# Optimization experiments

Hardware: AMD Instinct MI355X
Metric: run time of the kernel (lower is better)

Reference implementation:

```python
import jax, jax.numpy as jnp
import numpy as np

EPS = 1e-5

def conv1x1_bn(x, W, b, gamma, beta, mean, var):
    # x: (B,C,H,W); W: (O,C) 1x1 conv; BN in eval mode with running stats
    y = jnp.einsum('bchw,oc->bohw', x, W) + b[None, :, None, None]
    scale = gamma / jnp.sqrt(var + EPS)
    return y * scale[None, :, None, None] + (beta - mean * scale)[None, :, None, None]

def setup_inputs() -> dict:
    key = jax.random.key(0)
    ks = jax.random.split(key, 12)
    B, C, H, W = 8, 64, 128, 256
    d = {
        'fea_left': jax.random.normal(ks[0], (B, C, H, W), jnp.float32),
        'fea_right': jax.random.normal(ks[1], (B, C, H, W), jnp.float32),
        'Wq': jax.random.normal(ks[2], (C, C), jnp.float32) * (1.0 / np.sqrt(C)),
        'bq': jax.random.normal(ks[3], (C,), jnp.float32) * 0.02,
        'gq': 1.0 + 0.1 * jax.random.normal(ks[4], (C,), jnp.float32),
        'betaq': 0.02 * jax.random.normal(ks[5], (C,), jnp.float32),
        'mq': 0.02 * jax.random.normal(ks[6], (C,), jnp.float32),
        'vq': jax.random.uniform(ks[7], (C,), jnp.float32, 0.5, 1.5),
        'Wk': jax.random.normal(ks[8], (C, C), jnp.float32) * (1.0 / np.sqrt(C)),
        'bk': jax.random.normal(ks[9], (C,), jnp.float32) * 0.02,
        'gk': 1.0 + 0.1 * jax.random.normal(ks[10], (C,), jnp.float32),
        'betak': 0.02 * jax.random.normal(ks[11], (C,), jnp.float32),
        'mk': 0.02 * jax.random.normal(jax.random.fold_in(key, 100), (C,), jnp.float32),
        'vk': jax.random.uniform(jax.random.fold_in(key, 101), (C,), jnp.float32, 0.5, 1.5),
    }
    return d

def _attend(src, tgt, Wq, bq, gq, betaq, mq, vq, Wk, bk, gk, betak, mk, vk):
    # query from src, key from tgt, values are raw tgt features
    c = src.shape[1]
    Q = conv1x1_bn(src, Wq, bq, gq, betaq, mq, vq)   # (B,C,H,W)
    K = conv1x1_bn(tgt, Wk, bk, gk, betak, mk, vk)   # (B,C,H,W)
    # cost: (B,H,Wq,Wk) = Q^T K over channels, per image row
    cost = jnp.einsum('bchw,bchv->bhwv', Q, K) / c
    attn = jax.nn.softmax(cost, axis=-1)
    out = jnp.einsum('bhwv,bchv->bchw', attn, tgt)   # back to (B,C,H,W)
    return out

def reference(fea_left, fea_right, Wq, bq, gq, betaq, mq, vq, Wk, bk, gk, betak, mk, vk):
    cxr = _attend(fea_left, fea_right, Wq, bq, gq, betaq, mq, vq, Wk, bk, gk, betak, mk, vk)
    enh = _attend(fea_right, fea_left, Wq, bq, gq, betaq, mq, vq, Wk, bk, gk, betak, mk, vk)
    return (cxr, enh)
```

## Files before the change

kernel.cpp:

```cpp
#include <hip/hip_runtime.h>

#define HW_ 32768
#define OUTHALF 16777216ULL
#define SMEM_BYTES 117760

typedef short short8  __attribute__((ext_vector_type(8)));
typedef short short4v __attribute__((ext_vector_type(4)));
typedef float f32x4   __attribute__((ext_vector_type(4)));

__device__ __forceinline__ unsigned short f2bf(float f) {
  unsigned u = __builtin_bit_cast(unsigned, f);
  u += 0x7fffu + ((u >> 16) & 1u);
  return (unsigned short)(u >> 16);
}
__device__ __forceinline__ float bf2f(short s) {
  unsigned u = ((unsigned)(unsigned short)s) << 16;
  return __builtin_bit_cast(float, u);
}
__device__ __forceinline__ char* swz(char* base, int row, int colByte) {
  return base + row * 128 + (colByte ^ ((row & 7) << 4));
}
__device__ __forceinline__ f32x4 zero4() { f32x4 z = {0.f, 0.f, 0.f, 0.f}; return z; }

__global__ void pam_setup(const float* __restrict__ Wq, const float* __restrict__ bq,
                          const float* __restrict__ gq, const float* __restrict__ betaq,
                          const float* __restrict__ mq, const float* __restrict__ vq,
                          const float* __restrict__ Wk, const float* __restrict__ gk,
                          const float* __restrict__ vk,
                          short* __restrict__ Mbt, float* __restrict__ u) {
  int blk = blockIdx.x, tid = threadIdx.x;
  if (blk < 16) {
    int entry = blk * 256 + tid;
    int y = entry >> 6, x = entry & 63;
    float acc = 0.f;
    for (int o = 0; o < 64; ++o) {
      float sq = gq[o] * rsqrtf(vq[o] + 1e-5f);
      float sk = gk[o] * rsqrtf(vk[o] + 1e-5f);
      acc += Wq[o * 64 + x] * sq * Wk[o * 64 + y] * sk;
    }
    Mbt[y * 64 + x] = (short)f2bf(acc);
  } else if (tid < 64) {
    int y = tid;
    float acc = 0.f;
    for (int o = 0; o < 64; ++o) {
      float sq = gq[o] * rsqrtf(vq[o] + 1e-5f);
      float sk = gk[o] * rsqrtf(vk[o] + 1e-5f);
      float bqq = bq[o] * sq + betaq[o] - mq[o] * sq;
      acc += bqq * Wk[o * 64 + y] * sk;
    }
    u[y] = acc;
  }
}

__global__ __launch_bounds__(1024, 4) void pam_main(
    const float* __restrict__ fl, const float* __restrict__ fr,
    const short* __restrict__ Mbt, const float* __restrict__ uvec,
    float* __restrict__ out) {
  extern __shared__ __align__(16) char sm[];
  char* XLt = sm;
  char* XRt = sm + 32768;
  char* Xn0 = sm + 65536;
  char* Pt  = sm + 81920;
  float* tl = (float*)(sm + 114688);
  float* Db = (float*)(sm + 116736);

  const int tid  = threadIdx.x;
  const int lane = tid & 63;
  const int wave = tid >> 6;
  const int l15  = lane & 15;
  const int g    = lane >> 4;
  const int bb   = blockIdx.x >> 7;
  const int hh   = blockIdx.x & 127;
  const int rowOff = hh * 256;
  const int base_b = bb * 64;
  const int w0   = wave * 16;

  char* Ptw = Pt + wave * 2048;

  #pragma unroll
  for (int it = 0; it < 8; ++it) {
    int unit = it * 1024 + tid;
    int tensor = unit >> 12;
    int rem = unit & 4095;
    int cq = rem >> 8;
    int p  = rem & 255;
    const float* s = (tensor ? fr : fl) + (size_t)(base_b + cq * 4) * HW_ + rowOff + p;
    float v0 = s[0], v1 = s[HW_], v2 = s[2 * HW_], v3 = s[3 * HW_];
    short4v pk;
    pk[0] = (short)f2bf(v0); pk[1] = (short)f2bf(v1);
    pk[2] = (short)f2bf(v2); pk[3] = (short)f2bf(v3);
    *(short4v*)swz(tensor ? XRt : XLt, p, cq * 8) = pk;
  }
  __syncthreads();

  if (tid < 512) {
    int sel = tid >> 8, p = tid & 255;
    char* xt = sel ? XLt : XRt;
    float acc = 0.f;
    #pragma unroll
    for (int j = 0; j < 8; ++j) {
      short8 xv = *(const short8*)swz(xt, p, j * 16);
      #pragma unroll
      for (int e = 0; e < 8; ++e)
        acc = fmaf(bf2f(xv[e]), uvec[j * 8 + e], acc);
    }
    tl[sel * 256 + p] = acc * 0.015625f;
  }

  #pragma unroll 1
  for (int at = 0; at < 2; ++at) {
    char* Xq  = at ? XRt : XLt;
    char* Xkv = at ? XLt : XRt;
    const float* skv = at ? fl : fr;
    const float* tp  = tl + at * 256;
    float* outp = out + (at ? OUTHALF : 0) + (size_t)base_b * HW_ + rowOff;

    short8 bq_[2];
    {
      short8 xb_[2];
      #pragma unroll
      for (int kk = 0; kk < 2; ++kk)
        xb_[kk] = *(const short8*)swz(Xq, w0 + l15, (kk * 32 + 8 * g) * 2);
      #pragma unroll
      for (int mi = 0; mi < 4; ++mi) {
        f32x4 q = zero4();
        #pragma unroll
        for (int kk = 0; kk < 2; ++kk) {
          short8 am = *(const short8*)(Mbt + (mi * 16 + l15) * 64 + kk * 32 + 8 * g);
          q = __builtin_amdgcn_mfma_f32_16x16x32_bf16(am, xb_[kk], q, 0, 0, 0);
        }
        short4v p4;
        p4[0] = (short)f2bf(q[0]); p4[1] = (short)f2bf(q[1]);
        p4[2] = (short)f2bf(q[2]); p4[3] = (short)f2bf(q[3]);
        *(short4v*)swz(Ptw, l15, mi * 32 + 8 * g) = p4;
      }
      #pragma unroll
      for (int kk = 0; kk < 2; ++kk)
        bq_[kk] = *(const short8*)swz(Ptw, l15, kk * 64 + 16 * g);
    }

    f32x4 acc_o[4];
    #pragma unroll
    for (int j = 0; j < 4; ++j) acc_o[j] = zero4();
    float dacc = 0.f;

    const int vc = tid >> 4;
    const int v4 = (tid & 15) * 4;
    const float* vbase = skv + (size_t)(base_b + vc) * HW_ + rowOff + v4;
    f32x4 A0 = *(const f32x4*)vbase;
    {
      short4v pk;
      pk[0] = (short)f2bf(A0[0]); pk[1] = (short)f2bf(A0[1]);
      pk[2] = (short)f2bf(A0[2]); pk[3] = (short)f2bf(A0[3]);
      *(short4v*)swz(Xn0, vc, v4 * 2) = pk;
    }
    A0 = *(const f32x4*)(vbase + 64);
    __syncthreads();

    for (int vt = 0; vt < 4; ++vt) {
      if (vt < 3) {
        short4v pk;
        pk[0] = (short)f2bf(A0[0]); pk[1] = (short)f2bf(A0[1]);
        pk[2] = (short)f2bf(A0[2]); pk[3] = (short)f2bf(A0[3]);
        *(short4v*)swz(Xn0 + ((vt + 1) & 1) * 8192, vc, v4 * 2) = pk;
      }
      if (vt < 2) A0 = *(const f32x4*)(vbase + (vt + 2) * 64);
      char* XnB = Xn0 + (vt & 1) * 8192;

      f32x4 accs[4];
      #pragma unroll
      for (int mi = 0; mi < 4; ++mi) {
        accs[mi] = zero4();
        #pragma unroll
        for (int kk = 0; kk < 2; ++kk) {
          short8 af = *(const short8*)swz(Xkv, vt * 64 + mi * 16 + l15,
                                          (kk * 32 + 8 * g) * 2);
          accs[mi] = __builtin_amdgcn_mfma_f32_16x16x32_bf16(af, bq_[kk], accs[mi], 0, 0, 0);
        }
      }
      #pragma unroll
      for (int mi = 0; mi < 4; ++mi) {
        f32x4 tr = *(const f32x4*)(tp + vt * 64 + mi * 16 + 4 * g);
        f32x4 pv;
        #pragma unroll
        for (int r = 0; r < 4; ++r)
          pv[r] = __expf(fmaf(accs[mi][r], 0.015625f, tr[r]));
        dacc += pv[0] + pv[1] + pv[2] + pv[3];
        short4v p4;
        p4[0] = (short)f2bf(pv[0]); p4[1] = (short)f2bf(pv[1]);
        p4[2] = (short)f2bf(pv[2]); p4[3] = (short)f2bf(pv[3]);
        *(short4v*)swz(Ptw, l15, mi * 32 + 8 * g) = p4;
      }
      #pragma unroll
      for (int kk = 0; kk < 2; ++kk) {
        short8 pa = *(const short8*)swz(Ptw, l15, kk * 64 + 16 * g);
        #pragma unroll
        for (int nj2 = 0; nj2 < 4; ++nj2) {
          short8 xb = *(const short8*)swz(XnB, nj2 * 16 + l15, (kk * 32 + 8 * g) * 2);
          acc_o[nj2] = __builtin_amdgcn_mfma_f32_16x16x32_bf16(pa, xb, acc_o[nj2], 0, 0, 0);
        }
      }
      __syncthreads();
    }

    dacc += __shfl_xor(dacc, 16); dacc += __shfl_xor(dacc, 32);
    if (lane < 16) Db[wave * 16 + lane] = __builtin_amdgcn_rcpf(dacc);
    f32x4 rd = *(const f32x4*)(Db + wave * 16 + 4 * g);
    #pragma unroll
    for (int nj2 = 0; nj2 < 4; ++nj2) {
      int c = nj2 * 16 + l15;
      f32x4 v;
      v[0] = acc_o[nj2][0] * rd[0];
      v[1] = acc_o[nj2][1] * rd[1];
      v[2] = acc_o[nj2][2] * rd[2];
      v[3] = acc_o[nj2][3] * rd[3];
      *(f32x4*)(outp + (size_t)c * HW_ + w0 + 4 * g) = v;
    }
  }
}

extern "C" void kernel_launch(void* const* d_in, const int* in_sizes, int n_in,
                              void* d_out, int out_size, void* d_ws, size_t ws_size,
                              hipStream_t stream) {
  (void)in_sizes; (void)n_in; (void)out_size; (void)ws_size;
  const float* fl    = (const float*)d_in[0];
  const float* fr    = (const float*)d_in[1];
  const float* Wq    = (const float*)d_in[2];
  const float* bq    = (const float*)d_in[3];
  const float* gq    = (const float*)d_in[4];
  const float* betaq = (const float*)d_in[5];
  const float* mq    = (const float*)d_in[6];
  const float* vq    = (const float*)d_in[7];
  const float* Wk    = (const float*)d_in[8];
  const float* gk    = (const float*)d_in[10];
  const float* vk    = (const float*)d_in[13];
  short* Mbt = (short*)d_ws;
  float* u   = (float*)((char*)d_ws + 8192);
  float* out = (float*)d_out;

  hipFuncSetAttribute((const void*)pam_main,
                      hipFuncAttributeMaxDynamicSharedMemorySize, SMEM_BYTES);
  pam_setup<<<17, 256, 0, stream>>>(Wq, bq, gq, betaq, mq, vq, Wk, gk, vk, Mbt, u);
  pam_main<<<1024, 1024, SMEM_BYTES, stream>>>(fl, fr, Mbt, u, out);
}
```

Baseline: 127.7 us.

## Transpose MFMA fragments via lane shuffles instead of LDS staging; single-buffer V

```diff
diff --git a/kernel.cpp b/kernel.cpp
--- a/kernel.cpp
+++ b/kernel.cpp
@@ -2,11 +2,12 @@
 
 #define HW_ 32768
 #define OUTHALF 16777216ULL
-#define SMEM_BYTES 117760
+#define SMEM_BYTES 76800
 
 typedef short short8  __attribute__((ext_vector_type(8)));
 typedef short short4v __attribute__((ext_vector_type(4)));
 typedef float f32x4   __attribute__((ext_vector_type(4)));
+typedef unsigned int uint4v __attribute__((ext_vector_type(4)));
 
 __device__ __forceinline__ unsigned short f2bf(float f) {
   unsigned u = __builtin_bit_cast(unsigned, f);
@@ -17,10 +18,44 @@
   unsigned u = ((unsigned)(unsigned short)s) << 16;
   return __builtin_bit_cast(float, u);
 }
+__device__ __forceinline__ unsigned pkw(float lo, float hi) {
+  return ((unsigned)f2bf(hi) << 16) | (unsigned)f2bf(lo);
+}
 __device__ __forceinline__ char* swz(char* base, int row, int colByte) {
   return base + row * 128 + (colByte ^ ((row & 7) << 4));
 }
 __device__ __forceinline__ f32x4 zero4() { f32x4 z = {0.f, 0.f, 0.f, 0.f}; return z; }
+
+__device__ __forceinline__ void xpose(const f32x4 (&p)[4], int g,
+                                      short8& f0, short8& f1) {
+  unsigned W00 = pkw(p[0][0], p[0][1]), W01 = pkw(p[0][2], p[0][3]);
+  unsigned W10 = pkw(p[1][0], p[1][1]), W11 = pkw(p[1][2], p[1][3]);
+  unsigned W20 = pkw(p[2][0], p[2][1]), W21 = pkw(p[2][2], p[2][3]);
+  unsigned W30 = pkw(p[3][0], p[3][1]), W31 = pkw(p[3][2], p[3][3]);
+  const bool h2 = (g & 2) != 0;
+  unsigned SA0 = h2 ? W10 : W00, SA1 = h2 ? W11 : W01;
+  unsigned SA2 = h2 ? W30 : W20, SA3 = h2 ? W31 : W21;
+  unsigned SB0 = h2 ? W00 : W10, SB1 = h2 ? W01 : W11;
+  unsigned SB2 = h2 ? W20 : W30, SB3 = h2 ? W21 : W31;
+  unsigned ra0 = __shfl_xor((int)SA0, 16), ra1 = __shfl_xor((int)SA1, 16);
+  unsigned ra2 = __shfl_xor((int)SA2, 16), ra3 = __shfl_xor((int)SA3, 16);
+  unsigned rb0 = __shfl_xor((int)SB0, 32), rb1 = __shfl_xor((int)SB1, 32);
+  unsigned rb2 = __shfl_xor((int)SB2, 32), rb3 = __shfl_xor((int)SB3, 32);
+  unsigned rc0 = __shfl_xor((int)SB0, 48), rc1 = __shfl_xor((int)SB1, 48);
+  unsigned rc2 = __shfl_xor((int)SB2, 48), rc3 = __shfl_xor((int)SB3, 48);
+  unsigned a0 = g==0 ? SA0 : g==1 ? rc0 : g==2 ? rb0 : ra0;
+  unsigned a1 = g==0 ? SA1 : g==1 ? rc1 : g==2 ? rb1 : ra1;
+  unsigned a2 = g==0 ? SA2 : g==1 ? rc2 : g==2 ? rb2 : ra2;
+  unsigned a3 = g==0 ? SA3 : g==1 ? rc3 : g==2 ? rb3 : ra3;
+  unsigned b0 = g==3 ? SA0 : g==2 ? rc0 : g==1 ? rb0 : ra0;
+  unsigned b1 = g==3 ? SA1 : g==2 ? rc1 : g==1 ? rb1 : ra1;
+  unsigned b2 = g==3 ? SA2 : g==2 ? rc2 : g==1 ? rb2 : ra2;
+  unsigned b3 = g==3 ? SA3 : g==2 ? rc3 : g==1 ? rb3 : ra3;
+  uint4v u0 = {a0, a1, b0, b1};
+  uint4v u1 = {a2, a3, b2, b3};
+  f0 = __builtin_bit_cast(short8, u0);
+  f1 = __builtin_bit_cast(short8, u1);
+}
 
 __global__ void pam_setup(const float* __restrict__ Wq, const float* __restrict__ bq,
                           const float* __restrict__ gq, const float* __restrict__ betaq,
@@ -52,17 +87,16 @@
   }
 }
 
-__global__ __launch_bounds__(1024, 4) void pam_main(
+__global__ __launch_bounds__(1024, 8) void pam_main(
     const float* __restrict__ fl, const float* __restrict__ fr,
     const short* __restrict__ Mbt, const float* __restrict__ uvec,
     float* __restrict__ out) {
   extern __shared__ __align__(16) char sm[];
   char* XLt = sm;
   char* XRt = sm + 32768;
-  char* Xn0 = sm + 65536;
-  char* Pt  = sm + 81920;
-  float* tl = (float*)(sm + 114688);
-  float* Db = (float*)(sm + 116736);
+  char* Xn  = sm + 65536;
+  float* tl = (float*)(sm + 73728);
+  float* Db = (float*)(sm + 75776);
 
   const int tid  = threadIdx.x;
   const int lane = tid & 63;
@@ -74,8 +108,6 @@
   const int rowOff = hh * 256;
   const int base_b = bb * 64;
   const int w0   = wave * 16;
-
-  char* Ptw = Pt + wave * 2048;
 
   #pragma unroll
   for (int it = 0; it < 8; ++it) {
@@ -107,6 +139,9 @@
     tl[sel * 256 + p] = acc * 0.015625f;
   }
 
+  const int vc = tid >> 4;
+  const int v4 = (tid & 15) * 4;
+
   #pragma unroll 1
   for (int at = 0; at < 2; ++at) {
     char* Xq  = at ? XRt : XLt;
@@ -117,26 +152,18 @@
 
     short8 bq_[2];
     {
-      short8 xb_[2];
-      #pragma unroll
-      for (int kk = 0; kk < 2; ++kk)
-        xb_[kk] = *(const short8*)swz(Xq, w0 + l15, (kk * 32 + 8 * g) * 2);
+      short8 xb0 = *(const short8*)swz(Xq, w0 + l15, (8 * g) * 2);
+      short8 xb1 = *(const short8*)swz(Xq, w0 + l15, (32 + 8 * g) * 2);
+      f32x4 qa[4];
       #pragma unroll
       for (int mi = 0; mi < 4; ++mi) {
-        f32x4 q = zero4();
-        #pragma unroll
-        for (int kk = 0; kk < 2; ++kk) {
-          short8 am = *(const short8*)(Mbt + (mi * 16 + l15) * 64 + kk * 32 + 8 * g);
-          q = __builtin_amdgcn_mfma_f32_16x16x32_bf16(am, xb_[kk], q, 0, 0, 0);
-        }
-        short4v p4;
-        p4[0] = (short)f2bf(q[0]); p4[1] = (short)f2bf(q[1]);
-        p4[2] = (short)f2bf(q[2]); p4[3] = (short)f2bf(q[3]);
-        *(short4v*)swz(Ptw, l15, mi * 32 + 8 * g) = p4;
-      }
-      #pragma unroll
-      for (int kk = 0; kk < 2; ++kk)
-        bq_[kk] = *(const short8*)swz(Ptw, l15, kk * 64 + 16 * g);
+        qa[mi] = zero4();
+        short8 am0 = *(const short8*)(Mbt + (mi * 16 + l15) * 64 + 8 * g);
+        short8 am1 = *(const short8*)(Mbt + (mi * 16 + l15) * 64 + 32 + 8 * g);
+        qa[mi] = __builtin_amdgcn_mfma_f32_16x16x32_bf16(am0, xb0, qa[mi], 0, 0, 0);
+        qa[mi] = __builtin_amdgcn_mfma_f32_16x16x32_bf16(am1, xb1, qa[mi], 0, 0, 0);
+      }
+      xpose(qa, g, bq_[0], bq_[1]);
     }
 
     f32x4 acc_o[4];
@@ -144,63 +171,59 @@
     for (int j = 0; j < 4; ++j) acc_o[j] = zero4();
     float dacc = 0.f;
 
-    const int vc = tid >> 4;
-    const int v4 = (tid & 15) * 4;
     const float* vbase = skv + (size_t)(base_b + vc) * HW_ + rowOff + v4;
     f32x4 A0 = *(const f32x4*)vbase;
     {
       short4v pk;
       pk[0] = (short)f2bf(A0[0]); pk[1] = (short)f2bf(A0[1]);
       pk[2] = (short)f2bf(A0[2]); pk[3] = (short)f2bf(A0[3]);
-      *(short4v*)swz(Xn0, vc, v4 * 2) = pk;
+      *(short4v*)swz(Xn, vc, v4 * 2) = pk;
     }
     A0 = *(const f32x4*)(vbase + 64);
     __syncthreads();
 
+    short8 pf0, pf1;
+    auto mk_p = [&](int vt) {
+      f32x4 ps[4];
+      #pragma unroll
+      for (int mi = 0; mi < 4; ++mi) {
+        ps[mi] = zero4();
+        short8 af0 = *(const short8*)swz(Xkv, vt * 64 + mi * 16 + l15, (8 * g) * 2);
+        short8 af1 = *(const short8*)swz(Xkv, vt * 64 + mi * 16 + l15, (32 + 8 * g) * 2);
+        ps[mi] = __builtin_amdgcn_mfma_f32_16x16x32_bf16(af0, bq_[0], ps[mi], 0, 0, 0);
+        ps[mi] = __builtin_amdgcn_mfma_f32_16x16x32_bf16(af1, bq_[1], ps[mi], 0, 0, 0);
+      }
+      #pragma unroll
+      for (int mi = 0; mi < 4; ++mi) {
+        f32x4 tr = *(const f32x4*)(tp + vt * 64 + mi * 16 + 4 * g);
+        #pragma unroll
+        for (int r = 0; r < 4; ++r)
+          ps[mi][r] = __expf(fmaf(ps[mi][r], 0.015625f, tr[r]));
+        dacc += ps[mi][0] + ps[mi][1] + ps[mi][2] + ps[mi][3];
+      }
+      xpose(ps, g, pf0, pf1);
+    };
+
+    mk_p(0);
+    #pragma unroll
     for (int vt = 0; vt < 4; ++vt) {
+      #pragma unroll
+      for (int nj2 = 0; nj2 < 4; ++nj2) {
+        short8 xb0 = *(const short8*)swz(Xn, nj2 * 16 + l15, (8 * g) * 2);
+        short8 xb1 = *(const short8*)swz(Xn, nj2 * 16 + l15, (32 + 8 * g) * 2);
+        acc_o[nj2] = __builtin_amdgcn_mfma_f32_16x16x32_bf16(pf0, xb0, acc_o[nj2], 0, 0, 0);
+        acc_o[nj2] = __builtin_amdgcn_mfma_f32_16x16x32_bf16(pf1, xb1, acc_o[nj2], 0, 0, 0);
+      }
+      __syncthreads();
       if (vt < 3) {
         short4v pk;
         pk[0] = (short)f2bf(A0[0]); pk[1] = (short)f2bf(A0[1]);
         pk[2] = (short)f2bf(A0[2]); pk[3] = (short)f2bf(A0[3]);
-        *(short4v*)swz(Xn0 + ((vt + 1) & 1) * 8192, vc, v4 * 2) = pk;
-      }
-      if (vt < 2) A0 = *(const f32x4*)(vbase + (vt + 2) * 64);
-      char* XnB = Xn0 + (vt & 1) * 8192;
-
-      f32x4 accs[4];
-      #pragma unroll
-      for (int mi = 0; mi < 4; ++mi) {
-        accs[mi] = zero4();
-        #pragma unroll
-        for (int kk = 0; kk < 2; ++kk) {
-          short8 af = *(const short8*)swz(Xkv, vt * 64 + mi * 16 + l15,
-                                          (kk * 32 + 8 * g) * 2);
-          accs[mi] = __builtin_amdgcn_mfma_f32_16x16x32_bf16(af, bq_[kk], accs[mi], 0, 0, 0);
-        }
-      }
-      #pragma unroll
-      for (int mi = 0; mi < 4; ++mi) {
-        f32x4 tr = *(const f32x4*)(tp + vt * 64 + mi * 16 + 4 * g);
-        f32x4 pv;
-        #pragma unroll
-        for (int r = 0; r < 4; ++r)
-          pv[r] = __expf(fmaf(accs[mi][r], 0.015625f, tr[r]));
-        dacc += pv[0] + pv[1] + pv[2] + pv[3];
-        short4v p4;
-        p4[0] = (short)f2bf(pv[0]); p4[1] = (short)f2bf(pv[1]);
-        p4[2] = (short)f2bf(pv[2]); p4[3] = (short)f2bf(pv[3]);
-        *(short4v*)swz(Ptw, l15, mi * 32 + 8 * g) = p4;
-      }
-      #pragma unroll
-      for (int kk = 0; kk < 2; ++kk) {
-        short8 pa = *(const short8*)swz(Ptw, l15, kk * 64 + 16 * g);
-        #pragma unroll
-        for (int nj2 = 0; nj2 < 4; ++nj2) {
-          short8 xb = *(const short8*)swz(XnB, nj2 * 16 + l15, (kk * 32 + 8 * g) * 2);
-          acc_o[nj2] = __builtin_amdgcn_mfma_f32_16x16x32_bf16(pa, xb, acc_o[nj2], 0, 0, 0);
-        }
-      }
-      __syncthreads();
+        *(short4v*)swz(Xn, vc, v4 * 2) = pk;
+        if (vt < 2) A0 = *(const f32x4*)(vbase + (vt + 2) * 64);
+        mk_p(vt + 1);
+        __syncthreads();
+      }
     }
 
     dacc += __shfl_xor(dacc, 16); dacc += __shfl_xor(dacc, 32);
@@ -216,6 +239,7 @@
       v[3] = acc_o[nj2][3] * rd[3];
       *(f32x4*)(outp + (size_t)c * HW_ + w0 + 4 * g) = v;
     }
+    __syncthreads();
   }
 }
 
```

New measurement: 202.5 us. 1.59x slower.
